# Performance work log

Hardware: AMD Instinct MI355X
Metric: run time of the kernel (lower is better)

Reference implementation:

```python
import jax, jax.numpy as jnp
import numpy as np

K_SIZE = 5  # neighborhood window

def _extract_patches(x, k):
    # tf.image.extract_patches with stride 1, SAME (zero) padding.
    # x: [B,H,W,C] -> [B,H,W,k*k,C]
    pad = k // 2
    B, H, W, C = x.shape
    xp = jnp.pad(x, ((0, 0), (pad, pad), (pad, pad), (0, 0)))
    # fixed small k*k loop (25 shifted views), stacked along patch axis
    return jnp.stack([xp[:, i:i + H, j:j + W, :]
                      for i in range(k) for j in range(k)], axis=3)

def setup_inputs() -> dict:
    key = jax.random.key(0)
    k1, k2, k3 = jax.random.split(key, 3)
    B, H, W, C, BIN = 2, 256, 256, 32, 32
    return {
        "main": jax.random.normal(k1, (B, H, W, C), dtype=jnp.float32),
        "ref": jax.random.normal(k2, (B, H, W, C), dtype=jnp.float32),
        "ref_value": jax.random.normal(k3, (B, H, W, BIN), dtype=jnp.float32),
    }

def reference(main, ref, ref_value):
    # mode='dot': local-window dot-product attention
    ref_stacked = _extract_patches(ref, K_SIZE)          # [B,H,W,k*k,C]
    attn = jnp.einsum('bhwc,bhwkc->bhwk', main, ref_stacked)
    attn = jax.nn.softmax(attn, axis=-1)                 # [B,H,W,k*k]
    # aggregate_mode='weighted_sum'
    ref_value_stacked = _extract_patches(ref_value, K_SIZE)  # [B,H,W,k*k,bin]
    return jnp.einsum('bhwk,bhwki->bhwi', attn, ref_value_stacked)
```

## Files before the change

kernel.cpp:

```cpp
#include <hip/hip_runtime.h>
#include <hip/hip_fp16.h>


typedef float v2f __attribute__((ext_vector_type(2)));

template <int CTRL>
__device__ __forceinline__ float dpp_add(float x)
{
    const int y = __builtin_amdgcn_mov_dpp(__float_as_int(x), CTRL, 0xF, 0xF, true);
    return x + __int_as_float(y);
}

__device__ __forceinline__ unsigned pkh(float a, float b)
{
    const __half2 h = __float22half2_rn(make_float2(a, b));
    return __builtin_bit_cast(unsigned, h);
}

__device__ __forceinline__ v2f uph(unsigned u)
{
    const __half2 h = __builtin_bit_cast(__half2, u);
    const float2 f = __half22float2(h);
    return (v2f){f.x, f.y};
}

__device__ __forceinline__ uint4 pack8(const float4 f0, const float4 f1)
{
    return make_uint4(pkh(f0.x, f0.y), pkh(f0.z, f0.w),
                      pkh(f1.x, f1.y), pkh(f1.z, f1.w));
}

__global__ void __launch_bounds__(256)
local_attn_kernel(const float* __restrict__ main_p,
                  const float* __restrict__ ref_p,
                  const float* __restrict__ rv_p,
                  float* __restrict__ out_p)
{
    const int tid  = threadIdx.x;
    const int lane = tid & 63;
    const int wv   = tid >> 6;
    const int s    = lane & 3;
    const int pw   = lane >> 2;

    const int bid  = blockIdx.x;
    const int ct   = bid & 15;
    const int band = (bid >> 4) & 63;
    const int b    = bid >> 10;

    const int col0 = ct * 16;
    const int hb   = band * 4;
    const int ib   = b << 16;

    const int wcol = col0 + pw;
    const int prow = hb + wv;

    const float4* m4 = (const float4*)main_p;
    const float4* r4 = (const float4*)ref_p;
    const float4* v4 = (const float4*)rv_p;
    float4*       o4 = (float4*)out_p;

    __shared__ uint4 sm[2][160];

    const bool stg = (tid < 160);
    const float4* sp = r4;
    if (stg) {
        const int c  = (tid < 80) ? tid : tid - 80;
        const int lc = c >> 2, cs = c & 3;
        const int g  = min(max(col0 - 2 + lc, 0), 255);
        sp = ((tid < 80) ? r4 : v4) + (((ib + g) << 3) + 2 * cs);
    }

    float cmask[5];
#pragma unroll
    for (int j = 0; j < 5; ++j)
        cmask[j] = ((unsigned)(wcol + j - 2) < 256u) ? 1.0f : 0.0f;

    const float L2E = 1.44269504088896340736f;

    v2f mA, mB, mC, mD;
    {
        const int pbase = ((ib + prow * 256 + wcol) << 3) + 2 * s;
        const float4 t0 = m4[pbase];
        const float4 t1 = m4[pbase + 1];
        mA = (v2f){t0.x * L2E, t0.y * L2E};
        mB = (v2f){t0.z * L2E, t0.w * L2E};
        mC = (v2f){t1.x * L2E, t1.y * L2E};
        mD = (v2f){t1.z * L2E, t1.w * L2E};
    }
    v2f aA = {0.f, 0.f}, aB = {0.f, 0.f}, aC = {0.f, 0.f}, aD = {0.f, 0.f};
    float sum = 0.0f;

    if (stg) {
        const int roff = (min(max(hb - 2, 0), 255)) << 11;
        sm[0][tid] = pack8(sp[roff], sp[roff + 1]);
    }
    __syncthreads();

#pragma unroll 1
    for (int rr = 0; rr < 8; ++rr) {
        float4 f0, f1;
        const bool more = (rr < 7);
        if (more && stg) {
            const int roff = (min(max(hb + rr - 1, 0), 255)) << 11;
            f0 = sp[roff];
            f1 = sp[roff + 1];
        }

        if (rr >= wv && rr <= wv + 4) {
            const int   gr  = hb + rr - 2;
            const float rok = ((unsigned)gr < 256u) ? 1.0f : 0.0f;
            const uint4* bp = &sm[rr & 1][0];

#pragma unroll
            for (int j = 0; j < 5; ++j) {
                const uint4 uR = bp[lane + 4 * j];
                const uint4 uV = bp[80 + lane + 4 * j];
                const float mj = cmask[j] * rok;

                v2f p = mA * uph(uR.x);
                p = mB * uph(uR.y) + p;
                p = mC * uph(uR.z) + p;
                p = mD * uph(uR.w) + p;
                float sc = p.x + p.y;
                sc = dpp_add<0xB1>(sc);
                sc = dpp_add<0x4E>(sc);

                const float e = __builtin_exp2f(sc * mj);
                sum += e;
                const float t = e * mj;
                const v2f t2 = {t, t};
                aA = t2 * uph(uV.x) + aA;
                aB = t2 * uph(uV.y) + aB;
                aC = t2 * uph(uV.z) + aC;
                aD = t2 * uph(uV.w) + aD;
            }
        }

        if (more) {
            if (stg) sm[(rr + 1) & 1][tid] = pack8(f0, f1);
            __syncthreads();
        }
    }

    const float inv = 1.0f / sum;
    const int obase = ((ib + prow * 256 + wcol) << 3) + 2 * s;
    o4[obase]     = make_float4(aA.x * inv, aA.y * inv, aB.x * inv, aB.y * inv);
    o4[obase + 1] = make_float4(aC.x * inv, aC.y * inv, aD.x * inv, aD.y * inv);
}

extern "C" void kernel_launch(void* const* d_in, const int* in_sizes, int n_in,
                              void* d_out, int out_size, void* d_ws, size_t ws_size,
                              hipStream_t stream)
{
    const float* main_p = (const float*)d_in[0];
    const float* ref_p  = (const float*)d_in[1];
    const float* rv_p   = (const float*)d_in[2];
    float*       out_p  = (float*)d_out;

    const int npix   = in_sizes[0] / 32;
    const int blocks = npix / 64;
    local_attn_kernel<<<blocks, 256, 0, stream>>>(main_p, ref_p, rv_p, out_p);
}
```

Measured before the change: 102.6 us.

## Stage full 16x16 tile halo in shared memory, loop four rows per wave

Each block now covers a 16x16 pixel tile instead of a 4x16 band. It loads the whole 20x20 halo of ref and ref_value into shared memory once as fp16, with a single barrier, and each wave then processes four output rows in turn. This cuts halo over-fetch, since rows are reused across 16 outputs instead of 4, and removes the per-row double-buffer barriers. In exchange it uses about 51KB of LDS per block, which lowers occupancy, and it quarters the block count to 512, less than the GPU's CU count.

```diff
diff --git a/kernel.cpp b/kernel.cpp
--- a/kernel.cpp
+++ b/kernel.cpp
@@ -24,12 +24,6 @@
     return (v2f){f.x, f.y};
 }
 
-__device__ __forceinline__ uint4 pack8(const float4 f0, const float4 f1)
-{
-    return make_uint4(pkh(f0.x, f0.y), pkh(f0.z, f0.w),
-                      pkh(f1.x, f1.y), pkh(f1.z, f1.w));
-}
-
 __global__ void __launch_bounds__(256)
 local_attn_kernel(const float* __restrict__ main_p,
                   const float* __restrict__ ref_p,
@@ -43,78 +37,68 @@
     const int pw   = lane >> 2;
 
     const int bid  = blockIdx.x;
-    const int ct   = bid & 15;
-    const int band = (bid >> 4) & 63;
-    const int b    = bid >> 10;
-
-    const int col0 = ct * 16;
-    const int hb   = band * 4;
+    const int tx   = (bid & 15) * 16;
+    const int ty   = ((bid >> 4) & 15) * 16;
+    const int b    = bid >> 8;
     const int ib   = b << 16;
-
-    const int wcol = col0 + pw;
-    const int prow = hb + wv;
 
     const float4* m4 = (const float4*)main_p;
     const float4* r4 = (const float4*)ref_p;
     const float4* v4 = (const float4*)rv_p;
     float4*       o4 = (float4*)out_p;
 
-    __shared__ uint4 sm[2][160];
+    __shared__ uint4 sm[3200];
 
-    const bool stg = (tid < 160);
-    const float4* sp = r4;
-    if (stg) {
-        const int c  = (tid < 80) ? tid : tid - 80;
-        const int lc = c >> 2, cs = c & 3;
-        const int g  = min(max(col0 - 2 + lc, 0), 255);
-        sp = ((tid < 80) ? r4 : v4) + (((ib + g) << 3) + 2 * cs);
+    for (int c = tid; c < 3200; c += 256) {
+        const int  cc   = (c < 1600) ? c : c - 1600;
+        const int  cell = cc >> 2;
+        const int  cs   = cc & 3;
+        const int  hr   = cell / 20;
+        const int  hc   = cell - hr * 20;
+        const int  gy   = min(max(ty - 2 + hr, 0), 255);
+        const int  gx   = min(max(tx - 2 + hc, 0), 255);
+        const float4* p = (c < 1600) ? r4 : v4;
+        const int  base = ((ib + gy * 256 + gx) << 3) + 2 * cs;
+        const float4 f0 = p[base];
+        const float4 f1 = p[base + 1];
+        sm[c] = make_uint4(pkh(f0.x, f0.y), pkh(f0.z, f0.w),
+                           pkh(f1.x, f1.y), pkh(f1.z, f1.w));
     }
+    __syncthreads();
+
+    const float L2E = 1.44269504088896340736f;
 
     float cmask[5];
 #pragma unroll
     for (int j = 0; j < 5; ++j)
-        cmask[j] = ((unsigned)(wcol + j - 2) < 256u) ? 1.0f : 0.0f;
+        cmask[j] = ((unsigned)(tx + pw + j - 2) < 256u) ? 1.0f : 0.0f;
 
-    const float L2E = 1.44269504088896340736f;
+#pragma unroll 1
+    for (int pr4 = 0; pr4 < 4; ++pr4) {
+        const int pr   = wv * 4 + pr4;
+        const int gyp  = ty + pr;
+        const int pbase = ((ib + gyp * 256 + tx + pw) << 3) + 2 * s;
 
-    v2f mA, mB, mC, mD;
-    {
-        const int pbase = ((ib + prow * 256 + wcol) << 3) + 2 * s;
         const float4 t0 = m4[pbase];
         const float4 t1 = m4[pbase + 1];
-        mA = (v2f){t0.x * L2E, t0.y * L2E};
-        mB = (v2f){t0.z * L2E, t0.w * L2E};
-        mC = (v2f){t1.x * L2E, t1.y * L2E};
-        mD = (v2f){t1.z * L2E, t1.w * L2E};
-    }
-    v2f aA = {0.f, 0.f}, aB = {0.f, 0.f}, aC = {0.f, 0.f}, aD = {0.f, 0.f};
-    float sum = 0.0f;
+        const v2f mA = (v2f){t0.x * L2E, t0.y * L2E};
+        const v2f mB = (v2f){t0.z * L2E, t0.w * L2E};
+        const v2f mC = (v2f){t1.x * L2E, t1.y * L2E};
+        const v2f mD = (v2f){t1.z * L2E, t1.w * L2E};
 
-    if (stg) {
-        const int roff = (min(max(hb - 2, 0), 255)) << 11;
-        sm[0][tid] = pack8(sp[roff], sp[roff + 1]);
-    }
-    __syncthreads();
+        v2f aA = {0.f, 0.f}, aB = {0.f, 0.f}, aC = {0.f, 0.f}, aD = {0.f, 0.f};
+        float sum = 0.0f;
 
-#pragma unroll 1
-    for (int rr = 0; rr < 8; ++rr) {
-        float4 f0, f1;
-        const bool more = (rr < 7);
-        if (more && stg) {
-            const int roff = (min(max(hb + rr - 1, 0), 255)) << 11;
-            f0 = sp[roff];
-            f1 = sp[roff + 1];
-        }
-
-        if (rr >= wv && rr <= wv + 4) {
-            const int   gr  = hb + rr - 2;
-            const float rok = ((unsigned)gr < 256u) ? 1.0f : 0.0f;
-            const uint4* bp = &sm[rr & 1][0];
+#pragma unroll
+        for (int i = 0; i < 5; ++i) {
+            const int   hr  = pr + i;
+            const float rok = ((unsigned)(gyp + i - 2) < 256u) ? 1.0f : 0.0f;
+            const int   rb  = hr * 80 + pw * 4 + s;
 
 #pragma unroll
             for (int j = 0; j < 5; ++j) {
-                const uint4 uR = bp[lane + 4 * j];
-                const uint4 uV = bp[80 + lane + 4 * j];
+                const uint4 uR = sm[rb + j * 4];
+                const uint4 uV = sm[1600 + rb + j * 4];
                 const float mj = cmask[j] * rok;
 
                 v2f p = mA * uph(uR.x);
@@ -136,16 +120,10 @@
             }
         }
 
-        if (more) {
-            if (stg) sm[(rr + 1) & 1][tid] = pack8(f0, f1);
-            __syncthreads();
-        }
+        const float inv = 1.0f / sum;
+        o4[pbase]     = make_float4(aA.x * inv, aA.y * inv, aB.x * inv, aB.y * inv);
+        o4[pbase + 1] = make_float4(aC.x * inv, aC.y * inv, aD.x * inv, aD.y * inv);
     }
-
-    const float inv = 1.0f / sum;
-    const int obase = ((ib + prow * 256 + wcol) << 3) + 2 * s;
-    o4[obase]     = make_float4(aA.x * inv, aA.y * inv, aB.x * inv, aB.y * inv);
-    o4[obase + 1] = make_float4(aC.x * inv, aC.y * inv, aD.x * inv, aD.y * inv);
 }
 
 extern "C" void kernel_launch(void* const* d_in, const int* in_sizes, int n_in,
@@ -158,6 +136,6 @@
     float*       out_p  = (float*)d_out;
 
     const int npix   = in_sizes[0] / 32;
-    const int blocks = npix / 64;
+    const int blocks = npix / 256;
     local_attn_kernel<<<blocks, 256, 0, stream>>>(main_p, ref_p, rv_p, out_p);
 }
```

Result: slower. 106.2 us (+3.5%).
